# Performance work log

Hardware: AMD Instinct MI355X
Metric: run time of the kernel (lower is better)

Reference implementation:

```python
import jax, jax.numpy as jnp
import numpy as np

T, B, D, H = 512, 64, 1024, 1024


def setup_inputs() -> dict:
    key = jax.random.key(0)
    ks = jax.random.split(key, 7)
    stdv = 1.0 / np.sqrt(H)
    u = lambda k, shape: jax.random.uniform(k, shape, jnp.float32, -stdv, stdv)
    return {
        "x": jax.random.normal(ks[0], (T, B, D), jnp.float32),
        "h0": jax.random.normal(ks[1], (B, H), jnp.float32),
        "c0": jax.random.normal(ks[2], (B, H), jnp.float32),
        "w_ih": u(ks[3], (4 * H, D)),
        "b_ih": u(ks[4], (4 * H,)),
        "w_hh": u(ks[5], (4 * H, H)),
        "b_hh": u(ks[6], (4 * H,)),
    }


def reference(x, h0, c0, w_ih, b_ih, w_hh, b_hh):
    # Precompute input projection for all timesteps in one big GEMM: [T,B,4H]
    gates_x = jnp.einsum("tbd,gd->tbg", x, w_ih) + b_ih

    def step(carry, gx_t):
        h, c = carry
        gates = gx_t + h @ w_hh.T + b_hh  # [B, 4H]
        i_in, f_in, g_in, o_in = jnp.split(gates, 4, axis=1)
        i_t = jax.nn.sigmoid(i_in)
        f_t = jax.nn.sigmoid(f_in)
        g_t = jnp.tanh(g_in)
        o_t = jax.nn.sigmoid(o_in)
        c_t = f_t * c + i_t * g_t
        h_t = o_t * jnp.tanh(c_t)
        return (h_t, c_t), h_t

    (h_n, c_n), hs = jax.lax.scan(step, (h0, c0), gates_x)
    # output: [T, B, H]; final states: [B, H]
    return hs, h_n, c_n
```

## Files before the change

### kernel.cpp

```cpp
#include <hip/hip_runtime.h>

#define TT 512
#define NB 64
#define DD 1024
#define NG 4096

typedef __attribute__((ext_vector_type(8))) __bf16 bf16x8;
typedef __attribute__((ext_vector_type(4))) float f32x4;

#define WC_OFF   0ul
#define HT_OFF   16777216ul
#define FLG_OFF  (HT_OFF + 262144ul)
#define BIAS_OFF (FLG_OFF + 2048ul)
#define XBF_OFF  (BIAS_OFF + 16384ul)
#define WS_FULL  (XBF_OFF + 67108864ul)

__device__ __forceinline__ unsigned short f2bf(float f) {
  unsigned int u = __float_as_uint(f);
  u += 0x7fffu + ((u >> 16) & 1u);
  return (unsigned short)(u >> 16);
}

__global__ void prep_kernel(const float* __restrict__ x, const float* __restrict__ h0,
                            const float* __restrict__ w_ih, const float* __restrict__ b_ih,
                            const float* __restrict__ w_hh, const float* __restrict__ b_hh,
                            unsigned char* __restrict__ ws, int use_xbf) {
  unsigned short* Wc  = (unsigned short*)(ws + WC_OFF);
  unsigned short* ht  = (unsigned short*)(ws + HT_OFF);
  unsigned int* flg   = (unsigned int*)(ws + FLG_OFF);
  float* bias         = (float*)(ws + BIAS_OFF);
  unsigned short* xbf = (unsigned short*)(ws + XBF_OFF);
  long tid = (long)blockIdx.x * blockDim.x + threadIdx.x;
  long stride = (long)gridDim.x * blockDim.x;
  for (long i = tid; i < (long)NG * 2048; i += stride) {
    int r = (int)(i >> 11), k = (int)(i & 2047);
    float v = (k < 1024) ? w_ih[(long)r * 1024 + k] : w_hh[(long)r * 1024 + (k - 1024)];
    Wc[i] = f2bf(v);
  }
  for (long i = tid; i < NG; i += stride) bias[i] = b_ih[i] + b_hh[i];
  for (long i = tid; i < (long)NB * DD; i += stride) {
    int row = (int)(i >> 10), col = (int)(i & 1023);
    int bg = row >> 4, r = row & 15, cg = col >> 4, c = col & 15;
    ht[65536 + ((bg * 64 + cg) * 256 + r * 16 + c)] = f2bf(h0[i]);
  }
  for (long i = tid; i < 512; i += stride) flg[i] = 0;
  if (use_xbf) {
    for (long i = tid; i < (long)TT * NB * DD; i += stride) xbf[i] = f2bf(x[i]);
  }
}

#define MFMA16 __builtin_amdgcn_mfma_f32_16x16x32_bf16

__launch_bounds__(512, 2)
__global__ void lstm_kernel(const float* __restrict__ x, const float* __restrict__ c0,
                            float* __restrict__ out, unsigned char* __restrict__ ws,
                            int use_xbf) {
  __shared__ __align__(16) float red[2][8][16][68];
  __shared__ float bias_l[64];

  const unsigned short* Wc  = (const unsigned short*)(ws + WC_OFF);
  unsigned long long* hbq   = (unsigned long long*)(ws + HT_OFF);
  unsigned int* hb32        = (unsigned int*)(ws + HT_OFF);
  const unsigned long long* flgq = (const unsigned long long*)(ws + FLG_OFF);
  unsigned int* flg         = (unsigned int*)(ws + FLG_OFF);
  const float* bias         = (const float*)(ws + BIAS_OFF);
  const unsigned short* xbf = (const unsigned short*)(ws + XBF_OFF);

  const int tid = threadIdx.x;
  const int bg = blockIdx.x >> 6;
  const int cg = blockIdx.x & 63;
  const int m0 = bg << 4;
  const int j0 = cg << 4;
  const int wv = tid >> 6;
  const int lane = tid & 63;
  const int ln = lane & 15;
  const int lq = lane >> 4;

  bf16x8 wx[16], wh[16];
  {
    const int kx = wv * 128 + lq * 8;
#pragma unroll
    for (int g = 0; g < 4; ++g) {
      const unsigned short* wp = Wc + (long)(g * 1024 + j0 + ln) * 2048 + kx;
#pragma unroll
      for (int ks = 0; ks < 4; ++ks) {
        wx[g * 4 + ks] = *reinterpret_cast<const bf16x8*>(wp + ks * 32);
        wh[g * 4 + ks] = *reinterpret_cast<const bf16x8*>(wp + 1024 + ks * 32);
      }
    }
  }
  if (tid < 64) bias_l[tid] = bias[(tid >> 4) * 1024 + j0 + (tid & 15)];

  const int rrow = ((wv & 1) << 3) + (lane >> 3);
  const int jc   = lane & 7;
  float cr0 = 0.f, cr1 = 0.f;
  if (wv < 2) {
    const float2 cv = *(const float2*)(c0 + (long)(m0 + rrow) * DD + j0 + 2 * jc);
    cr0 = cv.x; cr1 = cv.y;
  }

  const long xbase = (long)(m0 + ln) * DD + wv * 128 + lq * 8;
  uint4 xcur[4];
  auto load_x = [&](int tt) {
    if (use_xbf) {
      const unsigned short* xp = xbf + (long)tt * (NB * DD) + xbase;
#pragma unroll
      for (int ks = 0; ks < 4; ++ks)
        xcur[ks] = *reinterpret_cast<const uint4*>(xp + ks * 32);
    } else {
      const float* xp = x + (long)tt * (NB * DD) + xbase;
#pragma unroll
      for (int ks = 0; ks < 4; ++ks) {
        float4 f0 = *reinterpret_cast<const float4*>(xp + ks * 32);
        float4 f1 = *reinterpret_cast<const float4*>(xp + ks * 32 + 4);
        uint4 pk;
        pk.x = (unsigned)f2bf(f0.x) | ((unsigned)f2bf(f0.y) << 16);
        pk.y = (unsigned)f2bf(f0.z) | ((unsigned)f2bf(f0.w) << 16);
        pk.z = (unsigned)f2bf(f1.x) | ((unsigned)f2bf(f1.y) << 16);
        pk.w = (unsigned)f2bf(f1.z) | ((unsigned)f2bf(f1.w) << 16);
        xcur[ks] = pk;
      }
    }
  };
  load_x(0);

  int qoff[4];
#pragma unroll
  for (int ks = 0; ks < 4; ++ks)
    qoff[ks] = ((bg * 64 + wv * 8 + 2 * ks + (lq >> 1)) * 64) + ln * 4 + (lq & 1) * 2;
  const int foff = bg * 64 + wv * 8 + (lane & 7);

#pragma unroll 1
  for (int t = 0; t < TT; ++t) {
    const int rb = t & 1;

    if (t > 0) {
      const unsigned tgt = (unsigned)t;
      while (true) {
        unsigned long long v = __hip_atomic_load(flgq + foff, __ATOMIC_RELAXED,
                                                 __HIP_MEMORY_SCOPE_AGENT);
        bool ok = ((unsigned)v >= tgt) && ((unsigned)(v >> 32) >= tgt);
        if (__all(ok)) break;
        __builtin_amdgcn_s_sleep(1);
      }
    }
    asm volatile("" ::: "memory");

    const unsigned long long* hp = hbq + (((t + 1) & 1) << 14);
    unsigned long long q[8];
#pragma unroll
    for (int ks = 0; ks < 4; ++ks) {
      q[2 * ks]     = __hip_atomic_load(hp + qoff[ks],     __ATOMIC_RELAXED, __HIP_MEMORY_SCOPE_AGENT);
      q[2 * ks + 1] = __hip_atomic_load(hp + qoff[ks] + 1, __ATOMIC_RELAXED, __HIP_MEMORY_SCOPE_AGENT);
    }

    f32x4 a0 = {0.f, 0.f, 0.f, 0.f}, a1 = a0, a2 = a0, a3 = a0;
#pragma unroll
    for (int ks = 0; ks < 4; ++ks) {
      bf16x8 af = __builtin_bit_cast(bf16x8, xcur[ks]);
      a0 = MFMA16(af, wx[ks],      a0, 0, 0, 0);
      a1 = MFMA16(af, wx[4 + ks],  a1, 0, 0, 0);
      a2 = MFMA16(af, wx[8 + ks],  a2, 0, 0, 0);
      a3 = MFMA16(af, wx[12 + ks], a3, 0, 0, 0);
    }
    if (wv >= 2 && t + 1 < TT) load_x(t + 1);

#pragma unroll
    for (int ks = 0; ks < 4; ++ks) {
      union { unsigned long long qq[2]; bf16x8 v; } uu;
      uu.qq[0] = q[2 * ks]; uu.qq[1] = q[2 * ks + 1];
      a0 = MFMA16(uu.v, wh[ks],      a0, 0, 0, 0);
      a1 = MFMA16(uu.v, wh[4 + ks],  a1, 0, 0, 0);
      a2 = MFMA16(uu.v, wh[8 + ks],  a2, 0, 0, 0);
      a3 = MFMA16(uu.v, wh[12 + ks], a3, 0, 0, 0);
    }

#pragma unroll
    for (int r = 0; r < 4; ++r) {
      float* rp = &red[rb][wv][lq * 4 + r][ln];
      rp[0] = a0[r]; rp[16] = a1[r]; rp[32] = a2[r]; rp[48] = a3[r];
    }

    asm volatile("s_waitcnt lgkmcnt(0)" ::: "memory");
    __builtin_amdgcn_s_barrier();
    __builtin_amdgcn_sched_barrier(0);

    if (wv < 2) {
      __builtin_amdgcn_s_setprio(1);
      float s00 = bias_l[2 * jc],      s01 = bias_l[2 * jc + 1];
      float s10 = bias_l[16 + 2 * jc], s11 = bias_l[16 + 2 * jc + 1];
      float s20 = bias_l[32 + 2 * jc], s21 = bias_l[32 + 2 * jc + 1];
      float s30 = bias_l[48 + 2 * jc], s31 = bias_l[48 + 2 * jc + 1];
#pragma unroll
      for (int w = 0; w < 8; ++w) {
        const float* rp = &red[rb][w][rrow][2 * jc];
        float2 v0 = *(const float2*)(rp);
        float2 v1 = *(const float2*)(rp + 16);
        float2 v2 = *(const float2*)(rp + 32);
        float2 v3 = *(const float2*)(rp + 48);
        s00 += v0.x; s01 += v0.y;
        s10 += v1.x; s11 += v1.y;
        s20 += v2.x; s21 += v2.y;
        s30 += v3.x; s31 += v3.y;
      }
      float ig0 = 1.f / (1.f + __expf(-s00)), ig1 = 1.f / (1.f + __expf(-s01));
      float fg0 = 1.f / (1.f + __expf(-s10)), fg1 = 1.f / (1.f + __expf(-s11));
      float gg0 = 1.f - 2.f / (__expf(2.f * s20) + 1.f);
      float gg1 = 1.f - 2.f / (__expf(2.f * s21) + 1.f);
      float og0 = 1.f / (1.f + __expf(-s30)), og1 = 1.f / (1.f + __expf(-s31));
      float cn0 = fg0 * cr0 + ig0 * gg0;
      float cn1 = fg1 * cr1 + ig1 * gg1;
      cr0 = cn0; cr1 = cn1;
      float hv0 = og0 * (1.f - 2.f / (__expf(2.f * cn0) + 1.f));
      float hv1 = og1 * (1.f - 2.f / (__expf(2.f * cn1) + 1.f));

      unsigned int pw = (unsigned)f2bf(hv0) | ((unsigned)f2bf(hv1) << 16);
      __hip_atomic_store(hb32 + (rb << 15) + (bg * 64 + cg) * 128 + rrow * 8 + jc, pw,
                         __ATOMIC_RELAXED, __HIP_MEMORY_SCOPE_AGENT);
      asm volatile("s_waitcnt vmcnt(0)" ::: "memory");
      if (lane == 0)
        __hip_atomic_store(flg + bg * 128 + 2 * cg + wv, (unsigned)(t + 1),
                           __ATOMIC_RELAXED, __HIP_MEMORY_SCOPE_AGENT);

      const long ho = (long)(m0 + rrow) * 1024 + j0 + 2 * jc;
      *(float2*)(out + (long)t * 65536 + ho) = make_float2(hv0, hv1);
      if (t == TT - 1) {
        *(float2*)(out + (long)TT * 65536 + ho) = make_float2(hv0, hv1);
        *(float2*)(out + (long)TT * 65536 + 65536 + ho) = make_float2(cn0, cn1);
      }
      __builtin_amdgcn_s_setprio(0);
      if (t + 1 < TT) load_x(t + 1);
    }
  }
}

extern "C" void kernel_launch(void* const* d_in, const int* in_sizes, int n_in,
                              void* d_out, int out_size, void* d_ws, size_t ws_size,
                              hipStream_t stream) {
  const float* x    = (const float*)d_in[0];
  const float* h0   = (const float*)d_in[1];
  const float* c0   = (const float*)d_in[2];
  const float* w_ih = (const float*)d_in[3];
  const float* b_ih = (const float*)d_in[4];
  const float* w_hh = (const float*)d_in[5];
  const float* b_hh = (const float*)d_in[6];
  float* out = (float*)d_out;
  unsigned char* ws = (unsigned char*)d_ws;
  int use_xbf = (ws_size >= WS_FULL) ? 1 : 0;

  hipLaunchKernelGGL(prep_kernel, dim3(2048), dim3(256), 0, stream,
                     x, h0, w_ih, b_ih, w_hh, b_hh, ws, use_xbf);

  void* args[] = { (void*)&x, (void*)&c0, (void*)&out, (void*)&ws, (void*)&use_xbf };
  hipLaunchCooperativeKernel(reinterpret_cast<void*>(lstm_kernel),
                             dim3(256), dim3(512), args, 0, stream);
}
```

Before: 2.977 ms.

## Reduce gate partials via LDS atomics and replicate per-wave step flags

```diff
diff --git a/kernel.cpp b/kernel.cpp
--- a/kernel.cpp
+++ b/kernel.cpp
@@ -11,7 +11,7 @@
 #define WC_OFF   0ul
 #define HT_OFF   16777216ul
 #define FLG_OFF  (HT_OFF + 262144ul)
-#define BIAS_OFF (FLG_OFF + 2048ul)
+#define BIAS_OFF (FLG_OFF + 16384ul)
 #define XBF_OFF  (BIAS_OFF + 16384ul)
 #define WS_FULL  (XBF_OFF + 67108864ul)
 
@@ -43,7 +43,7 @@
     int bg = row >> 4, r = row & 15, cg = col >> 4, c = col & 15;
     ht[65536 + ((bg * 64 + cg) * 256 + r * 16 + c)] = f2bf(h0[i]);
   }
-  for (long i = tid; i < 512; i += stride) flg[i] = 0;
+  for (long i = tid; i < 4096; i += stride) flg[i] = 0;
   if (use_xbf) {
     for (long i = tid; i < (long)TT * NB * DD; i += stride) xbf[i] = f2bf(x[i]);
   }
@@ -55,7 +55,7 @@
 __global__ void lstm_kernel(const float* __restrict__ x, const float* __restrict__ c0,
                             float* __restrict__ out, unsigned char* __restrict__ ws,
                             int use_xbf) {
-  __shared__ __align__(16) float red[2][8][16][68];
+  __shared__ __align__(16) float red[2][16][68];
   __shared__ float bias_l[64];
 
   const unsigned short* Wc  = (const unsigned short*)(ws + WC_OFF);
@@ -90,6 +90,11 @@
     }
   }
   if (tid < 64) bias_l[tid] = bias[(tid >> 4) * 1024 + j0 + (tid & 15)];
+  for (int i = tid; i < 2 * 16 * 64; i += 512) {
+    int b = i >> 10, row = (i >> 6) & 15, c = i & 63;
+    red[b][row][c] = bias[(c >> 4) * 1024 + j0 + (c & 15)];
+  }
+  __syncthreads();
 
   const int rrow = ((wv & 1) << 3) + (lane >> 3);
   const int jc   = lane & 7;
@@ -127,8 +132,8 @@
   int qoff[4];
 #pragma unroll
   for (int ks = 0; ks < 4; ++ks)
-    qoff[ks] = ((bg * 64 + wv * 8 + 2 * ks + (lq >> 1)) * 64) + ln * 4 + (lq & 1) * 2;
-  const int foff = bg * 64 + wv * 8 + (lane & 7);
+    qoff[ks] = (bg * 64 + wv * 8 + 2 * ks + (lq >> 1)) * 64 + ln * 4 + (lq & 1) * 2;
+  const int foff = (wv * 4 + bg) * 64 + wv * 8 + (lane & 7);
 
 #pragma unroll 1
   for (int t = 0; t < TT; ++t) {
@@ -136,13 +141,17 @@
 
     if (t > 0) {
       const unsigned tgt = (unsigned)t;
+      #define PLOAD() __hip_atomic_load(flgq + foff, __ATOMIC_RELAXED, __HIP_MEMORY_SCOPE_AGENT)
+      #define POK(v)  (((unsigned)(v) >= tgt) && ((unsigned)((v) >> 32) >= tgt))
+      unsigned long long p0 = PLOAD(), p1 = PLOAD(), p2 = PLOAD(), p3 = PLOAD();
       while (true) {
-        unsigned long long v = __hip_atomic_load(flgq + foff, __ATOMIC_RELAXED,
-                                                 __HIP_MEMORY_SCOPE_AGENT);
-        bool ok = ((unsigned)v >= tgt) && ((unsigned)(v >> 32) >= tgt);
-        if (__all(ok)) break;
-        __builtin_amdgcn_s_sleep(1);
-      }
+        if (__all(POK(p0))) break; p0 = PLOAD();
+        if (__all(POK(p1))) break; p1 = PLOAD();
+        if (__all(POK(p2))) break; p2 = PLOAD();
+        if (__all(POK(p3))) break; p3 = PLOAD();
+      }
+      #undef PLOAD
+      #undef POK
     }
     asm volatile("" ::: "memory");
 
@@ -177,8 +186,11 @@
 
 #pragma unroll
     for (int r = 0; r < 4; ++r) {
-      float* rp = &red[rb][wv][lq * 4 + r][ln];
-      rp[0] = a0[r]; rp[16] = a1[r]; rp[32] = a2[r]; rp[48] = a3[r];
+      float* rp = &red[rb][lq * 4 + r][ln];
+      atomicAdd(rp,      a0[r]);
+      atomicAdd(rp + 16, a1[r]);
+      atomicAdd(rp + 32, a2[r]);
+      atomicAdd(rp + 48, a3[r]);
     }
 
     asm volatile("s_waitcnt lgkmcnt(0)" ::: "memory");
@@ -187,27 +199,20 @@
 
     if (wv < 2) {
       __builtin_amdgcn_s_setprio(1);
-      float s00 = bias_l[2 * jc],      s01 = bias_l[2 * jc + 1];
-      float s10 = bias_l[16 + 2 * jc], s11 = bias_l[16 + 2 * jc + 1];
-      float s20 = bias_l[32 + 2 * jc], s21 = bias_l[32 + 2 * jc + 1];
-      float s30 = bias_l[48 + 2 * jc], s31 = bias_l[48 + 2 * jc + 1];
-#pragma unroll
-      for (int w = 0; w < 8; ++w) {
-        const float* rp = &red[rb][w][rrow][2 * jc];
-        float2 v0 = *(const float2*)(rp);
-        float2 v1 = *(const float2*)(rp + 16);
-        float2 v2 = *(const float2*)(rp + 32);
-        float2 v3 = *(const float2*)(rp + 48);
-        s00 += v0.x; s01 += v0.y;
-        s10 += v1.x; s11 += v1.y;
-        s20 += v2.x; s21 += v2.y;
-        s30 += v3.x; s31 += v3.y;
-      }
-      float ig0 = 1.f / (1.f + __expf(-s00)), ig1 = 1.f / (1.f + __expf(-s01));
-      float fg0 = 1.f / (1.f + __expf(-s10)), fg1 = 1.f / (1.f + __expf(-s11));
-      float gg0 = 1.f - 2.f / (__expf(2.f * s20) + 1.f);
-      float gg1 = 1.f - 2.f / (__expf(2.f * s21) + 1.f);
-      float og0 = 1.f / (1.f + __expf(-s30)), og1 = 1.f / (1.f + __expf(-s31));
+      const float2 v0 = *(const float2*)&red[rb][rrow][2 * jc];
+      const float2 v1 = *(const float2*)&red[rb][rrow][16 + 2 * jc];
+      const float2 v2 = *(const float2*)&red[rb][rrow][32 + 2 * jc];
+      const float2 v3 = *(const float2*)&red[rb][rrow][48 + 2 * jc];
+      *(float2*)&red[rb][rrow][2 * jc]      = *(const float2*)&bias_l[2 * jc];
+      *(float2*)&red[rb][rrow][16 + 2 * jc] = *(const float2*)&bias_l[16 + 2 * jc];
+      *(float2*)&red[rb][rrow][32 + 2 * jc] = *(const float2*)&bias_l[32 + 2 * jc];
+      *(float2*)&red[rb][rrow][48 + 2 * jc] = *(const float2*)&bias_l[48 + 2 * jc];
+      if (t + 1 < TT) load_x(t + 1);
+      float ig0 = 1.f / (1.f + __expf(-v0.x)), ig1 = 1.f / (1.f + __expf(-v0.y));
+      float fg0 = 1.f / (1.f + __expf(-v1.x)), fg1 = 1.f / (1.f + __expf(-v1.y));
+      float gg0 = 1.f - 2.f / (__expf(2.f * v2.x) + 1.f);
+      float gg1 = 1.f - 2.f / (__expf(2.f * v2.y) + 1.f);
+      float og0 = 1.f / (1.f + __expf(-v3.x)), og1 = 1.f / (1.f + __expf(-v3.y));
       float cn0 = fg0 * cr0 + ig0 * gg0;
       float cn1 = fg1 * cr1 + ig1 * gg1;
       cr0 = cn0; cr1 = cn1;
@@ -218,8 +223,8 @@
       __hip_atomic_store(hb32 + (rb << 15) + (bg * 64 + cg) * 128 + rrow * 8 + jc, pw,
                          __ATOMIC_RELAXED, __HIP_MEMORY_SCOPE_AGENT);
       asm volatile("s_waitcnt vmcnt(0)" ::: "memory");
-      if (lane == 0)
-        __hip_atomic_store(flg + bg * 128 + 2 * cg + wv, (unsigned)(t + 1),
+      if (lane < 8)
+        __hip_atomic_store(flg + (lane * 4 + bg) * 128 + 2 * cg + wv, (unsigned)(t + 1),
                            __ATOMIC_RELAXED, __HIP_MEMORY_SCOPE_AGENT);
 
       const long ho = (long)(m0 + rrow) * 1024 + j0 + 2 * jc;
@@ -229,7 +234,6 @@
         *(float2*)(out + (long)TT * 65536 + 65536 + ho) = make_float2(cn0, cn1);
       }
       __builtin_amdgcn_s_setprio(0);
-      if (t + 1 < TT) load_x(t + 1);
     }
   }
 }
```

After: 7.717 ms. 159% more time.
